# Kernel optimization log

Measured on AMD Instinct MI355X. Metric: run time of the kernel, lower is better.

## Reference

```python
import jax, jax.numpy as jnp
import numpy as np

B, S, D, H, F = 2, 2048, 1024, 16, 4096
DK = D // H
EPS = 1e-6


def _ln(x, g, b):
    mu = jnp.mean(x, axis=-1, keepdims=True)
    var = jnp.mean(jnp.square(x - mu), axis=-1, keepdims=True)
    return (x - mu) * jax.lax.rsqrt(var + EPS) * g + b


def setup_inputs() -> dict:
    key = jax.random.key(0)
    ks = jax.random.split(key, 8)
    sc = 0.02
    return {
        "x": jax.random.normal(ks[0], (B, S, D), jnp.float32),
        "wq": jax.random.normal(ks[1], (D, D), jnp.float32) * sc,
        "bq": jnp.zeros((D,), jnp.float32),
        "wk": jax.random.normal(ks[2], (D, D), jnp.float32) * sc,
        "bk": jnp.zeros((D,), jnp.float32),
        "wv": jax.random.normal(ks[3], (D, D), jnp.float32) * sc,
        "bv": jnp.zeros((D,), jnp.float32),
        "wo": jax.random.normal(ks[4], (D, D), jnp.float32) * sc,
        "bo": jnp.zeros((D,), jnp.float32),
        "w1": jax.random.normal(ks[5], (D, F), jnp.float32) * sc,
        "b1": jnp.zeros((F,), jnp.float32),
        "w2": jax.random.normal(ks[6], (F, D), jnp.float32) * sc,
        "b2": jnp.zeros((D,), jnp.float32),
        "g1": jnp.ones((D,), jnp.float32),
        "be1": jnp.zeros((D,), jnp.float32),
        "g2": jnp.ones((D,), jnp.float32),
        "be2": jnp.zeros((D,), jnp.float32),
    }


def reference(x, wq, bq, wk, bk, wv, bv, wo, bo, w1, b1, w2, b2, g1, be1, g2, be2):
    # Multi-head self-attention (no masks, eval-mode dropout = identity)
    q = (x @ wq + bq).reshape(B, S, H, DK)
    k = (x @ wk + bk).reshape(B, S, H, DK)
    v = (x @ wv + bv).reshape(B, S, H, DK)
    scale = 1.0 / (DK ** 0.5)
    score = jnp.einsum('bihd,bjhd->bhij', q, k) * scale  # [B,H,S,S]
    p = jax.nn.softmax(score, axis=-1)
    attn = jnp.einsum('bhij,bjhd->bihd', p, v).reshape(B, S, D)
    attn = attn @ wo + bo
    # residual + LayerNorm 1
    h = _ln(x + attn, g1, be1)
    # FFN (relu) + residual + LayerNorm 2
    ff = jax.nn.relu(h @ w1 + b1) @ w2 + b2
    return _ln(h + ff, g2, be2)
```

## Files before the change

### kernel.cpp

```cpp
#include <hip/hip_runtime.h>
#include <hip/hip_bf16.h>
#include <cmath>

typedef __bf16 bf16_t;
typedef __bf16 bf16x4 __attribute__((ext_vector_type(4)));
typedef __bf16 bf16x8 __attribute__((ext_vector_type(8)));
typedef float  f32x4  __attribute__((ext_vector_type(4)));

__device__ __forceinline__ void gld_lds16(const bf16_t* g, bf16_t* l) {
    __builtin_amdgcn_global_load_lds(
        (const __attribute__((address_space(1))) void*)g,
        (__attribute__((address_space(3))) void*)l,
        16, 0, 0);
}

struct PrepArgs {
    const float* w[6]; bf16_t* wt[6];
    int K[6], N[6], start[6];
    const float* x; bf16_t* xb; int castStart;
    const float* bq; const float* bk; float* bqkv; int biasStart;
};

__global__ __launch_bounds__(256) void prep(PrepArgs pa) {
    __shared__ float tile[32][33];
    const int bid = blockIdx.x, t = threadIdx.x;
    if (bid < pa.castStart) {
        int mi = 0;
#pragma unroll
        for (int i = 1; i < 6; i++) if (bid >= pa.start[i]) mi = i;
        const int tt  = bid - pa.start[mi];
        const int nbx = pa.N[mi] >> 5;
        const int n0 = (tt % nbx) * 32, k0 = (tt / nbx) * 32;
        const float* in = pa.w[mi];
        bf16_t* out = pa.wt[mi];
        const int K = pa.K[mi], N = pa.N[mi];
        const int tx = t & 31, ty = t >> 5;
#pragma unroll
        for (int i = 0; i < 4; i++) {
            int kk = ty + i * 8;
            tile[kk][tx] = in[(size_t)(k0 + kk) * N + n0 + tx];
        }
        __syncthreads();
#pragma unroll
        for (int i = 0; i < 4; i++) {
            int nn = ty + i * 8;
            out[(size_t)(n0 + nn) * K + k0 + tx] = (bf16_t)tile[tx][nn];
        }
    } else if (bid < pa.biasStart) {
        int i = (bid - pa.castStart) * 256 + t;
        f32x4 v = ((const f32x4*)pa.x)[i];
        bf16x4 o;
        o[0] = (bf16_t)v[0]; o[1] = (bf16_t)v[1]; o[2] = (bf16_t)v[2]; o[3] = (bf16_t)v[3];
        ((bf16x4*)pa.xb)[i] = o;
    } else {
#pragma unroll
        for (int j = 0; j < 8; j++) {
            int idx = t * 8 + j;
            pa.bqkv[idx] = idx < 1024 ? pa.bq[idx] : pa.bk[idx - 1024];
        }
    }
}

template<int MT>
__global__ __launch_bounds__(256) void gemm_bt(
    const bf16_t* __restrict__ A, const bf16_t* __restrict__ Bt,
    const float* __restrict__ bias,
    float* __restrict__ Cf, bf16_t* __restrict__ Cb,
    int M, int N, int lda, int Kloc, int relu, int nbn, int bias_row,
    long bt_bstride, long c_bstride) {
    constexpr int TM = MT * 32;
    __shared__ __attribute__((aligned(16))) bf16_t As[2][TM * 32];
    __shared__ __attribute__((aligned(16))) bf16_t Bs[2][128 * 32];
    const int tid  = threadIdx.x;
    const int lane = tid & 63;
    const int wave = tid >> 6;
    const int wm = wave & 1, wn = wave >> 1;
    const int kh = blockIdx.z;

    const int span  = 8 * nbn;
    const int group = blockIdx.x / span;
    const int rem   = blockIdx.x % span;
    const int bm    = group * 8 + (rem & 7);
    const int bn    = rem >> 3;

    const bf16_t* Bt_b = Bt + (size_t)blockIdx.y * bt_bstride;
    float*  Cf_b = Cf ? Cf + (size_t)blockIdx.y * c_bstride + (size_t)kh * M * N : nullptr;
    bf16_t* Cb_b = Cb ? Cb + (size_t)blockIdx.y * c_bstride : nullptr;
    const int koff = kh * Kloc;

    const int r4 = tid >> 2;
    const int kc = (tid & 3) * 8;
    const bf16_t* Ag = A    + (size_t)(bm * TM  + r4) * lda + koff + kc;
    const bf16_t* Bg = Bt_b + (size_t)(bn * 128 + r4) * lda + koff + kc;

    f32x4 acc[MT][4] = {};
    const int mrow = lane & 15;
    const int q8   = (lane >> 4) * 8;

    for (int k0 = 0; k0 < Kloc; k0 += 64) {
        __syncthreads();
#pragma unroll
        for (int hh = 0; hh < 2; hh++) {
#pragma unroll
            for (int i = 0; i < MT / 2; i++)
                gld_lds16(Ag + (size_t)(i * 64) * lda + k0 + hh * 32,
                          &As[hh][i * 64 * 32] + tid * 8);
            gld_lds16(Bg + k0 + hh * 32,                  &Bs[hh][0] + tid * 8);
            gld_lds16(Bg + (size_t)64 * lda + k0 + hh * 32, &Bs[hh][64 * 32] + tid * 8);
        }
        __syncthreads();

#pragma unroll
        for (int hh = 0; hh < 2; hh++) {
            bf16x8 af[MT], bfr[4];
#pragma unroll
            for (int mt = 0; mt < MT; mt++)
                af[mt] = *(const bf16x8*)(&As[hh][(wm * (MT * 16) + mt * 16 + mrow) * 32 + q8]);
#pragma unroll
            for (int nt = 0; nt < 4; nt++)
                bfr[nt] = *(const bf16x8*)(&Bs[hh][(wn * 64 + nt * 16 + mrow) * 32 + q8]);
#pragma unroll
            for (int mt = 0; mt < MT; mt++)
#pragma unroll
                for (int nt = 0; nt < 4; nt++)
                    acc[mt][nt] = __builtin_amdgcn_mfma_f32_16x16x32_bf16(
                        af[mt], bfr[nt], acc[mt][nt], 0, 0, 0);
        }
    }

    const int rq = (lane >> 4) * 4;
#pragma unroll
    for (int mt = 0; mt < MT; mt++) {
        int row0 = bm * TM + wm * (MT * 16) + mt * 16 + rq;
#pragma unroll
        for (int nt = 0; nt < 4; nt++) {
            int col = bn * 128 + wn * 64 + nt * 16 + mrow;
            float bvc = (bias && kh == 0 && !bias_row) ? bias[col] : 0.f;
#pragma unroll
            for (int r = 0; r < 4; r++) {
                float bb = (bias && kh == 0 && bias_row) ? bias[row0 + r] : bvc;
                float v = acc[mt][nt][r] + bb;
                if (relu) v = fmaxf(v, 0.f);
                size_t idx = (size_t)(row0 + r) * N + col;
                if (Cf_b) Cf_b[idx] = v;
                if (Cb_b) Cb_b[idx] = (bf16_t)v;
            }
        }
    }
}

__global__ __launch_bounds__(256) void flash_attn_mfma(
    const bf16_t* __restrict__ QKb,
    const bf16_t* __restrict__ Vtg,
    bf16_t* __restrict__ Outb) {
    __shared__ __attribute__((aligned(16))) bf16_t Qs[2 * 64 * 32];
    __shared__ __attribute__((aligned(16))) bf16_t Ks[2 * 64 * 32];
    __shared__ __attribute__((aligned(16))) bf16_t Vs[2 * 64 * 32];
    __shared__ __attribute__((aligned(16))) bf16_t Ps[64 * 72];
    const int t = threadIdx.x;
    const int lane = t & 63, wave = t >> 6;
    const int g = lane >> 4, cl = lane & 15;
    const int b = blockIdx.z, h = blockIdx.y, q0 = blockIdx.x * 64;
    const int RS = 2048;
    const bf16_t* Qg = QKb + (size_t)(b * 2048 + q0) * RS + h * 64;
    const bf16_t* Kg = QKb + (size_t)(b * 2048) * RS + 1024 + h * 64;
    const bf16_t* Vg = Vtg + ((size_t)b * 1024 + h * 64) * 2048;

    const int sr = t >> 2;
    const int sc = (t & 3) * 8;

    gld_lds16(Qg + (size_t)sr * RS + sc,      Qs + t * 8);
    gld_lds16(Qg + (size_t)sr * RS + 32 + sc, Qs + 4096 + t * 8);

    f32x4 Oacc[4] = {};
    f32x4 Lacc = {};
    bf16x8 ones;
#pragma unroll
    for (int j = 0; j < 8; j++) ones[j] = (bf16_t)1.0f;

    const int qrow_s = (wave * 16 + cl) * 32 + g * 8;
    const int prow_w = (wave * 16 + cl) * 72;
    const float C = 0.125f * 1.4426950408889634f;

    for (int kt = 0; kt < 2048; kt += 64) {
        __syncthreads();
        gld_lds16(Kg + (size_t)(kt + sr) * RS + sc,       Ks + t * 8);
        gld_lds16(Kg + (size_t)(kt + sr) * RS + 32 + sc,  Ks + 4096 + t * 8);
        gld_lds16(Vg + (size_t)sr * 2048 + kt + sc,       Vs + t * 8);
        gld_lds16(Vg + (size_t)sr * 2048 + kt + 32 + sc,  Vs + 4096 + t * 8);
        __syncthreads();

        f32x4 Sacc[4] = {};
#pragma unroll
        for (int ks = 0; ks < 2; ks++) {
            bf16x8 bq = *(const bf16x8*)(Qs + ks * 4096 + qrow_s);
#pragma unroll
            for (int mt = 0; mt < 4; mt++) {
                bf16x8 ak = *(const bf16x8*)(Ks + ks * 4096 + (mt * 16 + cl) * 32 + g * 8);
                Sacc[mt] = __builtin_amdgcn_mfma_f32_16x16x32_bf16(ak, bq, Sacc[mt], 0, 0, 0);
            }
        }

#pragma unroll
        for (int mt = 0; mt < 4; mt++) {
            bf16x4 p4;
#pragma unroll
            for (int r = 0; r < 4; r++)
                p4[r] = (bf16_t)__builtin_amdgcn_exp2f(Sacc[mt][r] * C);
            *(bf16x4*)(Ps + prow_w + mt * 16 + g * 4) = p4;
        }

#pragma unroll
        for (int ks = 0; ks < 2; ks++) {
            bf16x8 ap = *(const bf16x8*)(Ps + prow_w + ks * 32 + g * 8);
            Lacc = __builtin_amdgcn_mfma_f32_16x16x32_bf16(ap, ones, Lacc, 0, 0, 0);
#pragma unroll
            for (int nt = 0; nt < 4; nt++) {
                bf16x8 bv = *(const bf16x8*)(Vs + ks * 4096 + (nt * 16 + cl) * 32 + g * 8);
                Oacc[nt] = __builtin_amdgcn_mfma_f32_16x16x32_bf16(ap, bv, Oacc[nt], 0, 0, 0);
            }
        }
    }

#pragma unroll
    for (int r = 0; r < 4; r++) {
        float inv = 1.f / Lacc[r];
        int qrow = q0 + wave * 16 + g * 4 + r;
        size_t base = (size_t)(b * 2048 + qrow) * 1024 + h * 64;
#pragma unroll
        for (int nt = 0; nt < 4; nt++)
            Outb[base + nt * 16 + cl] = (bf16_t)(Oacc[nt][r] * inv);
    }
}

__global__ __launch_bounds__(256) void resid_ln3(const float* __restrict__ a,
                                                 const float* __restrict__ p0,
                                                 const float* __restrict__ p1,
                                                 const float* __restrict__ g,
                                                 const float* __restrict__ be,
                                                 float* __restrict__ outf,
                                                 bf16_t* __restrict__ outb) {
    const int row = blockIdx.x, t = threadIdx.x;
    const size_t base = (size_t)row * 1024;
    f32x4 v = ((const f32x4*)(a + base))[t] + ((const f32x4*)(p0 + base))[t];
    if (p1) v += ((const f32x4*)(p1 + base))[t];
    float sum = v[0] + v[1] + v[2] + v[3];
    float sq  = v[0] * v[0] + v[1] * v[1] + v[2] * v[2] + v[3] * v[3];
#pragma unroll
    for (int o = 1; o < 64; o <<= 1) {
        sum += __shfl_xor(sum, o);
        sq  += __shfl_xor(sq, o);
    }
    __shared__ float red[8];
    int wave = t >> 6, lane = t & 63;
    if (lane == 0) { red[wave] = sum; red[4 + wave] = sq; }
    __syncthreads();
    sum = red[0] + red[1] + red[2] + red[3];
    sq  = red[4] + red[5] + red[6] + red[7];
    float mu  = sum * (1.f / 1024.f);
    float var = sq * (1.f / 1024.f) - mu * mu;
    float rs  = rsqrtf(var + 1e-6f);
    f32x4 g4 = ((const f32x4*)g)[t];
    f32x4 b4 = ((const f32x4*)be)[t];
    f32x4 o = (v - mu) * rs * g4 + b4;
    ((f32x4*)(outf + base))[t] = o;
    if (outb) {
        bf16x4 ob;
        ob[0] = (bf16_t)o[0]; ob[1] = (bf16_t)o[1]; ob[2] = (bf16_t)o[2]; ob[3] = (bf16_t)o[3];
        ((bf16x4*)(outb + base))[t] = ob;
    }
}

extern "C" void kernel_launch(void* const* d_in, const int* in_sizes, int n_in,
                              void* d_out, int out_size, void* d_ws, size_t ws_size,
                              hipStream_t stream) {
    (void)in_sizes; (void)n_in; (void)out_size; (void)ws_size;
    const float* x   = (const float*)d_in[0];
    const float* wq  = (const float*)d_in[1];
    const float* bq  = (const float*)d_in[2];
    const float* wk  = (const float*)d_in[3];
    const float* bk  = (const float*)d_in[4];
    const float* wv  = (const float*)d_in[5];
    const float* bv  = (const float*)d_in[6];
    const float* wo  = (const float*)d_in[7];
    const float* bo  = (const float*)d_in[8];
    const float* w1  = (const float*)d_in[9];
    const float* b1  = (const float*)d_in[10];
    const float* w2  = (const float*)d_in[11];
    const float* b2  = (const float*)d_in[12];
    const float* g1  = (const float*)d_in[13];
    const float* be1 = (const float*)d_in[14];
    const float* g2  = (const float*)d_in[15];
    const float* be2 = (const float*)d_in[16];
    float* out = (float*)d_out;

    char* ws = (char*)d_ws;
    const size_t MB = 1ull << 20;
    bf16_t* xb    = (bf16_t*)(ws + 0);
    bf16_t* WtQKV = (bf16_t*)(ws + 8 * MB);
    bf16_t* WtO   = (bf16_t*)(ws + 14 * MB);
    bf16_t* Wt1   = (bf16_t*)(ws + 16 * MB);
    bf16_t* Wt2   = (bf16_t*)(ws + 24 * MB);
    float*  bqkv  = (float*)(ws + 32 * MB);
    bf16_t* QKb   = (bf16_t*)(ws + 33 * MB);
    bf16_t* Vt    = (bf16_t*)(ws + 49 * MB);
    bf16_t* ffb   = (bf16_t*)(ws + 33 * MB);
    float*  oa    = (float*)(ws + 65 * MB);
    float*  f2    = (float*)(ws + 65 * MB);
    float*  hbuf  = (float*)(ws + 97 * MB);
    bf16_t* hb    = (bf16_t*)(ws + 113 * MB);
    bf16_t* ab    = xb;
    const int MN = 4096 * 1024;

    PrepArgs pa;
    pa.w[0] = wq; pa.w[1] = wk; pa.w[2] = wv; pa.w[3] = wo; pa.w[4] = w1; pa.w[5] = w2;
    pa.wt[0] = WtQKV; pa.wt[1] = WtQKV + 1024 * 1024; pa.wt[2] = WtQKV + 2048 * 1024;
    pa.wt[3] = WtO; pa.wt[4] = Wt1; pa.wt[5] = Wt2;
    int Ks[6] = {1024, 1024, 1024, 1024, 1024, 4096};
    int Ns[6] = {1024, 1024, 1024, 1024, 4096, 1024};
    int st[6] = {0, 1024, 2048, 3072, 4096, 8192};
    for (int i = 0; i < 6; i++) { pa.K[i] = Ks[i]; pa.N[i] = Ns[i]; pa.start[i] = st[i]; }
    pa.x = x; pa.xb = xb; pa.castStart = 12288;
    pa.bq = bq; pa.bk = bk; pa.bqkv = bqkv; pa.biasStart = 12288 + 4096;
    prep<<<12288 + 4096 + 1, 256, 0, stream>>>(pa);

    gemm_bt<4><<<512, 256, 0, stream>>>(xb, WtQKV, bqkv, nullptr, QKb,
                                        4096, 2048, 1024, 1024, 0, 16, 0, 0, 0);
    gemm_bt<2><<<dim3(256, 2, 1), 256, 0, stream>>>(WtQKV + 2048 * 1024, xb, bv,
                                        nullptr, Vt, 1024, 2048, 1024, 1024, 0, 16, 1,
                                        (long)2048 * 1024, (long)1024 * 2048);
    flash_attn_mfma<<<dim3(32, 16, 2), 256, 0, stream>>>(QKb, Vt, ab);
    gemm_bt<4><<<dim3(256, 1, 2), 256, 0, stream>>>(ab, WtO, bo, oa, nullptr,
                                        4096, 1024, 1024, 512, 0, 8, 0, 0, 0);
    resid_ln3<<<4096, 256, 0, stream>>>(x, oa, oa + MN, g1, be1, hbuf, hb);
    gemm_bt<4><<<1024, 256, 0, stream>>>(hb, Wt1, b1, nullptr, ffb,
                                         4096, 4096, 1024, 1024, 1, 32, 0, 0, 0);
    gemm_bt<4><<<dim3(256, 1, 2), 256, 0, stream>>>(ffb, Wt2, b2, f2, nullptr,
                                        4096, 1024, 4096, 2048, 0, 8, 0, 0, 0);
    resid_ln3<<<4096, 256, 0, stream>>>(hbuf, f2, f2 + MN, g2, be2, out, nullptr);
}
```

Baseline: 412.8 us.

## Double-buffer K/V tiles in flash attention, keep Q in registers, swizzle P

The attention kernel now prefetches the next K/V tile into a second LDS buffer while the current one is consumed, using one barrier per iteration instead of two. The goal is to hide global-to-LDS load latency behind the MFMA work. Q fragments are loaded once into registers rather than staged through LDS. The P scratch tile drops its 72-element padded rows for an XOR-swizzled 64-wide layout to avoid LDS bank conflicts. The LDS buffers are also resized to match the 2048-element halves actually indexed, which removes the earlier over-indexing of Qs/Ks/Vs. The double buffering costs extra LDS per block and relies on the barrier waiting for the async LDS loads to finish.

```diff
diff --git a/kernel.cpp b/kernel.cpp
--- a/kernel.cpp
+++ b/kernel.cpp
@@ -153,10 +153,9 @@
     const bf16_t* __restrict__ QKb,
     const bf16_t* __restrict__ Vtg,
     bf16_t* __restrict__ Outb) {
-    __shared__ __attribute__((aligned(16))) bf16_t Qs[2 * 64 * 32];
-    __shared__ __attribute__((aligned(16))) bf16_t Ks[2 * 64 * 32];
-    __shared__ __attribute__((aligned(16))) bf16_t Vs[2 * 64 * 32];
-    __shared__ __attribute__((aligned(16))) bf16_t Ps[64 * 72];
+    __shared__ __attribute__((aligned(16))) bf16_t Ks[2][4096];
+    __shared__ __attribute__((aligned(16))) bf16_t Vs[2][4096];
+    __shared__ __attribute__((aligned(16))) bf16_t Ps[4096];
     const int t = threadIdx.x;
     const int lane = t & 63, wave = t >> 6;
     const int g = lane >> 4, cl = lane & 15;
@@ -169,8 +168,15 @@
     const int sr = t >> 2;
     const int sc = (t & 3) * 8;
 
-    gld_lds16(Qg + (size_t)sr * RS + sc,      Qs + t * 8);
-    gld_lds16(Qg + (size_t)sr * RS + 32 + sc, Qs + 4096 + t * 8);
+    const bf16_t* Qrow = Qg + (size_t)(wave * 16 + cl) * RS;
+    bf16x8 qr0 = *(const bf16x8*)(Qrow + g * 8);
+    bf16x8 qr1 = *(const bf16x8*)(Qrow + 32 + g * 8);
+
+    gld_lds16(Kg + (size_t)sr * RS + sc,        &Ks[0][0]    + t * 8);
+    gld_lds16(Kg + (size_t)sr * RS + 32 + sc,   &Ks[0][2048] + t * 8);
+    gld_lds16(Vg + (size_t)sr * 2048 + sc,      &Vs[0][0]    + t * 8);
+    gld_lds16(Vg + (size_t)sr * 2048 + 32 + sc, &Vs[0][2048] + t * 8);
+    __syncthreads();
 
     f32x4 Oacc[4] = {};
     f32x4 Lacc = {};
@@ -178,48 +184,54 @@
 #pragma unroll
     for (int j = 0; j < 8; j++) ones[j] = (bf16_t)1.0f;
 
-    const int qrow_s = (wave * 16 + cl) * 32 + g * 8;
-    const int prow_w = (wave * 16 + cl) * 72;
+    const int rowb = wave * 16 + cl;
+    const int psw  = (cl & 7) << 4;
+    char* PsB = (char*)Ps;
     const float C = 0.125f * 1.4426950408889634f;
 
-    for (int kt = 0; kt < 2048; kt += 64) {
-        __syncthreads();
-        gld_lds16(Kg + (size_t)(kt + sr) * RS + sc,       Ks + t * 8);
-        gld_lds16(Kg + (size_t)(kt + sr) * RS + 32 + sc,  Ks + 4096 + t * 8);
-        gld_lds16(Vg + (size_t)sr * 2048 + kt + sc,       Vs + t * 8);
-        gld_lds16(Vg + (size_t)sr * 2048 + kt + 32 + sc,  Vs + 4096 + t * 8);
-        __syncthreads();
+    for (int kt_i = 0; kt_i < 32; ++kt_i) {
+        const int cur = kt_i & 1;
+        if (kt_i + 1 < 32) {
+            const int nb  = cur ^ 1;
+            const int ktn = (kt_i + 1) * 64;
+            gld_lds16(Kg + (size_t)(ktn + sr) * RS + sc,        &Ks[nb][0]    + t * 8);
+            gld_lds16(Kg + (size_t)(ktn + sr) * RS + 32 + sc,   &Ks[nb][2048] + t * 8);
+            gld_lds16(Vg + (size_t)sr * 2048 + ktn + sc,        &Vs[nb][0]    + t * 8);
+            gld_lds16(Vg + (size_t)sr * 2048 + ktn + 32 + sc,   &Vs[nb][2048] + t * 8);
+        }
 
         f32x4 Sacc[4] = {};
 #pragma unroll
-        for (int ks = 0; ks < 2; ks++) {
-            bf16x8 bq = *(const bf16x8*)(Qs + ks * 4096 + qrow_s);
-#pragma unroll
-            for (int mt = 0; mt < 4; mt++) {
-                bf16x8 ak = *(const bf16x8*)(Ks + ks * 4096 + (mt * 16 + cl) * 32 + g * 8);
+        for (int ks = 0; ks < 2; ++ks) {
+            bf16x8 bq = ks ? qr1 : qr0;
+#pragma unroll
+            for (int mt = 0; mt < 4; ++mt) {
+                bf16x8 ak = *(const bf16x8*)(&Ks[cur][ks * 2048 + (mt * 16 + cl) * 32 + g * 8]);
                 Sacc[mt] = __builtin_amdgcn_mfma_f32_16x16x32_bf16(ak, bq, Sacc[mt], 0, 0, 0);
             }
         }
 
 #pragma unroll
-        for (int mt = 0; mt < 4; mt++) {
+        for (int mt = 0; mt < 4; ++mt) {
             bf16x4 p4;
 #pragma unroll
             for (int r = 0; r < 4; r++)
                 p4[r] = (bf16_t)__builtin_amdgcn_exp2f(Sacc[mt][r] * C);
-            *(bf16x4*)(Ps + prow_w + mt * 16 + g * 4) = p4;
-        }
-
-#pragma unroll
-        for (int ks = 0; ks < 2; ks++) {
-            bf16x8 ap = *(const bf16x8*)(Ps + prow_w + ks * 32 + g * 8);
+            *(bf16x4*)(PsB + ((rowb * 128 + mt * 32 + g * 8) ^ psw)) = p4;
+        }
+
+#pragma unroll
+        for (int ks = 0; ks < 2; ++ks) {
+            bf16x8 ap = *(const bf16x8*)(PsB + ((rowb * 128 + ks * 64 + g * 16) ^ psw));
             Lacc = __builtin_amdgcn_mfma_f32_16x16x32_bf16(ap, ones, Lacc, 0, 0, 0);
 #pragma unroll
-            for (int nt = 0; nt < 4; nt++) {
-                bf16x8 bv = *(const bf16x8*)(Vs + ks * 4096 + (nt * 16 + cl) * 32 + g * 8);
+            for (int nt = 0; nt < 4; ++nt) {
+                bf16x8 bv = *(const bf16x8*)(&Vs[cur][ks * 2048 + (nt * 16 + cl) * 32 + g * 8]);
                 Oacc[nt] = __builtin_amdgcn_mfma_f32_16x16x32_bf16(ap, bv, Oacc[nt], 0, 0, 0);
             }
         }
+
+        __syncthreads();
     }
 
 #pragma unroll
```

New measurement: 414.7 us. Within noise of the previous version (+0.4%).
